# Performance work log

Hardware: AMD Instinct MI355X
Metric: run time of the kernel (lower is better)

Reference implementation:

```python
import jax, jax.numpy as jnp
import numpy as np

N = 100000      # nodes
E = 1600000     # edges (before self loops)
F_IN = 128
HID = 32
H = 4
OUT = 32
NEG_SLOPE = 0.2


def setup_inputs() -> dict:
    key = jax.random.key(0)
    ks = jax.random.split(key, 10)
    x = jax.random.normal(ks[0], (N, F_IN), jnp.float32)
    edge_index = jax.random.randint(ks[1], (2, E), 0, N, jnp.int32)
    s1 = 1.0 / np.sqrt(F_IN)
    s2 = 1.0 / np.sqrt(H * HID)
    W1 = jax.random.normal(ks[2], (F_IN, H * HID), jnp.float32) * s1
    a_src1 = jax.random.normal(ks[3], (H, HID), jnp.float32) * 0.1
    a_dst1 = jax.random.normal(ks[4], (H, HID), jnp.float32) * 0.1
    b1 = jnp.zeros((H * HID,), jnp.float32)
    W2 = jax.random.normal(ks[5], (H * HID, OUT), jnp.float32) * s2
    a_src2 = jax.random.normal(ks[6], (1, OUT), jnp.float32) * 0.1
    a_dst2 = jax.random.normal(ks[7], (1, OUT), jnp.float32) * 0.1
    b2 = jnp.zeros((OUT,), jnp.float32)
    return {"x": x, "edge_index": edge_index, "W1": W1, "a_src1": a_src1,
            "a_dst1": a_dst1, "b1": b1, "W2": W2, "a_src2": a_src2,
            "a_dst2": a_dst2, "b2": b2}


def gat_conv(x, src, dst, W, a_src, a_dst, b, heads, out_ch):
    # PyG GATConv (concat=True) with self loops already appended to src/dst.
    n = x.shape[0]
    h = (x @ W).reshape(n, heads, out_ch)                 # [N,H,C]
    alpha_s = jnp.sum(h * a_src, axis=-1)                 # [N,H]
    alpha_d = jnp.sum(h * a_dst, axis=-1)                 # [N,H]
    e = jax.nn.leaky_relu(alpha_s[src] + alpha_d[dst], NEG_SLOPE)  # [E',H]
    # segment softmax over destination nodes (self loops => every segment nonempty)
    emax = jax.ops.segment_max(e, dst, num_segments=n)
    ex = jnp.exp(e - emax[dst])
    denom = jax.ops.segment_sum(ex, dst, num_segments=n)
    alpha = ex / denom[dst]                               # [E',H]
    msg = h[src] * alpha[:, :, None]                      # [E',H,C]
    out = jax.ops.segment_sum(msg, dst, num_segments=n)   # [N,H,C]
    return out.reshape(n, heads * out_ch) + b


def reference(x, edge_index, W1, a_src1, a_dst1, b1, W2, a_src2, a_dst2, b2):
    loops = jnp.arange(N, dtype=edge_index.dtype)
    src = jnp.concatenate([edge_index[0], loops])
    dst = jnp.concatenate([edge_index[1], loops])
    h = gat_conv(x, src, dst, W1, a_src1, a_dst1, b1, H, HID)
    h = jax.nn.relu(h)                                    # dropout: eval mode, no-op
    out = gat_conv(h, src, dst, W2, a_src2, a_dst2, b2, 1, OUT)
    return out
```

## Files before the change

kernel.cpp:

```cpp
#include <hip/hip_runtime.h>
#include <hip/hip_fp16.h>

#define NEG 0.2f
#define EPB 4096
#define BSH 6
#define SLOT 48
#define CAP 1280
#define KBMAX 1664
#define SRCBITS 20
#define SRCMASK 0xFFFFFu

typedef _Float16 half8 __attribute__((ext_vector_type(8)));
typedef float f32x4 __attribute__((ext_vector_type(4)));

__device__ inline __half2 pun_h2(float f) { union { float f; __half2 h; } u; u.f = f; return u.h; }
__device__ inline float pun_f(__half2 h) { union { float f; __half2 h; } u; u.h = h; return u.f; }

__global__ void k_prep(const float* __restrict__ W1, const float* __restrict__ W2,
                       half8* __restrict__ Wp, half8* __restrict__ W2p,
                       int* __restrict__ gcount, int KB) {
    int b = blockIdx.x;
    if (b < 8) {
        int u = b * 256 + threadIdx.x;
        int s = u >> 9, tn = (u >> 6) & 7, lane = u & 63;
        int quad = lane >> 4, c = lane & 15;
        half8 v;
#pragma unroll
        for (int j = 0; j < 8; ++j)
            v[j] = (_Float16)W1[(s * 32 + quad * 8 + j) * 128 + tn * 16 + c];
        Wp[u] = v;
    } else if (b < 10) {
        int u = (b - 8) * 256 + threadIdx.x;
        int n = u >> 8, s = (u >> 6) & 3, lane = u & 63;
        int quad = lane >> 4, c = lane & 15;
        half8 v;
#pragma unroll
        for (int j = 0; j < 8; ++j)
            v[j] = (_Float16)W2[(s * 32 + quad * 8 + j) * 32 + n * 16 + c];
        W2p[u] = v;
    } else {
        int i = (b - 10) * 256 + threadIdx.x;
        if (i < KB) gcount[i] = 0;
    }
}

__global__ __launch_bounds__(256) void k_pA(const float* __restrict__ x,
                                            const half8* __restrict__ Wp,
                                            const float* __restrict__ a_s,
                                            const float* __restrict__ a_d,
                                            __half* __restrict__ h1h,
                                            float* __restrict__ as1,
                                            float* __restrict__ ad1, int N,
                                            const int* __restrict__ srcp,
                                            const int* __restrict__ dstp,
                                            int* __restrict__ gcount,
                                            unsigned* __restrict__ ebuf,
                                            int E, int KB, int ngemm) {
    __shared__ _Float16 xa[64][136];
    __shared__ int lh[KBMAX];
    int t = threadIdx.x;

    if (blockIdx.x >= ngemm) {
        int blk = blockIdx.x - ngemm;
        int base0 = blk * EPB;
        int ss[16], dd[16];
#pragma unroll
        for (int j = 0; j < 16; ++j) {
            int i = base0 + j * 256 + t;
            if (i < E) { ss[j] = srcp[i]; dd[j] = dstp[i]; } else dd[j] = -1;
        }
        for (int i = t; i < KB; i += 256) lh[i] = 0;
        __syncthreads();
#pragma unroll
        for (int j = 0; j < 16; ++j)
            if (dd[j] >= 0) atomicAdd(&lh[dd[j] >> BSH], 1);
        __syncthreads();
        for (int b = t; b < KB; b += 256) {
            int c = lh[b];
            if (c > 0) lh[b] = atomicAdd(&gcount[b], c);
        }
        __syncthreads();
#pragma unroll
        for (int j = 0; j < 16; ++j) {
            if (dd[j] >= 0) {
                int b = dd[j] >> BSH;
                int pos = atomicAdd(&lh[b], 1);
                ebuf[(size_t)b * CAP + pos] =
                    (unsigned)ss[j] | ((unsigned)(dd[j] & 63) << SRCBITS);
            }
        }
        return;
    }

    int row0 = blockIdx.x * 64;
    {
        int row = t >> 2;
        int col0 = (t & 3) * 32;
        int gr = row0 + row;
        const float4* xsrc = (const float4*)&x[(size_t)gr * 128 + col0];
#pragma unroll
        for (int m = 0; m < 4; ++m) {
            float4 p0, p1;
            if (gr < N) { p0 = xsrc[m * 2]; p1 = xsrc[m * 2 + 1]; }
            else { p0 = float4{0,0,0,0}; p1 = float4{0,0,0,0}; }
            half8 v;
            v[0] = (_Float16)p0.x; v[1] = (_Float16)p0.y;
            v[2] = (_Float16)p0.z; v[3] = (_Float16)p0.w;
            v[4] = (_Float16)p1.x; v[5] = (_Float16)p1.y;
            v[6] = (_Float16)p1.z; v[7] = (_Float16)p1.w;
            *(half8*)&xa[row][col0 + m * 8] = v;
        }
    }
    __syncthreads();

    int w = t >> 6;
    int lane = t & 63;
    int quad = lane >> 4, c = lane & 15;

    f32x4 acc[8];
#pragma unroll
    for (int i = 0; i < 8; ++i) acc[i] = f32x4{0, 0, 0, 0};

#pragma unroll
    for (int s = 0; s < 4; ++s) {
        half8 a = *(const half8*)&xa[w * 16 + c][s * 32 + quad * 8];
#pragma unroll
        for (int tn = 0; tn < 8; ++tn) {
            half8 b = Wp[(s * 8 + tn) * 64 + lane];
            acc[tn] = __builtin_amdgcn_mfma_f32_16x16x32_f16(a, b, acc[tn], 0, 0, 0);
        }
    }

    float asv[8], adv[8];
#pragma unroll
    for (int tn = 0; tn < 8; ++tn) { asv[tn] = a_s[tn * 16 + c]; adv[tn] = a_d[tn * 16 + c]; }
#pragma unroll
    for (int r = 0; r < 4; ++r) {
        int gr = row0 + w * 16 + quad * 4 + r;
#pragma unroll
        for (int h = 0; h < 4; ++h) {
            float ps = acc[2*h][r] * asv[2*h] + acc[2*h+1][r] * asv[2*h+1];
            float pd = acc[2*h][r] * adv[2*h] + acc[2*h+1][r] * adv[2*h+1];
            ps += __shfl_xor(ps, 1); ps += __shfl_xor(ps, 2);
            ps += __shfl_xor(ps, 4); ps += __shfl_xor(ps, 8);
            pd += __shfl_xor(pd, 1); pd += __shfl_xor(pd, 2);
            pd += __shfl_xor(pd, 4); pd += __shfl_xor(pd, 8);
            if (c == 0 && gr < N) { as1[gr * 4 + h] = ps; ad1[gr * 4 + h] = pd; }
        }
    }

    __syncthreads();
#pragma unroll
    for (int tn = 0; tn < 8; ++tn)
#pragma unroll
        for (int r = 0; r < 4; ++r)
            xa[w * 16 + quad * 4 + r][tn * 16 + c] = (_Float16)acc[tn][r];
    __syncthreads();
    {
        int row = t >> 2;
        int seg = t & 3;
        int gr = row0 + row;
        if (gr < N) {
            float4* gp = (float4*)&h1h[(size_t)gr * 128 + seg * 32];
#pragma unroll
            for (int i = 0; i < 4; ++i)
                gp[i] = *(float4*)&xa[row][seg * 32 + i * 8];
        }
    }
}

__global__ __launch_bounds__(256) void k_aggC(const unsigned* __restrict__ ebuf,
                                              const int* __restrict__ gcount,
                                              const __half* __restrict__ h1h,
                                              const float* __restrict__ as1,
                                              const float* __restrict__ ad1,
                                              const float* __restrict__ b1,
                                              const half8* __restrict__ W2p,
                                              const float* __restrict__ asw,
                                              const float* __restrict__ adw,
                                              __half* __restrict__ h2h,
                                              float* __restrict__ as2,
                                              float* __restrict__ ad2, int N) {
    __shared__ int lcnt[64];
    __shared__ int lcsr[64 * SLOT];
    __shared__ _Float16 stg[4][16][136];
    int t = threadIdx.x;
    int b = blockIdx.x, d0 = b << BSH;

    if (t < 64) lcnt[t] = 0;
    __syncthreads();

    int ecnt = gcount[b];
    const unsigned* eb = &ebuf[(size_t)b * CAP];
    for (int i = t; i < ecnt; i += 256) {
        unsigned e = eb[i];
        int li = e >> SRCBITS;
        int r = atomicAdd(&lcnt[li], 1);
        lcsr[li * SLOT + r] = (int)(e & SRCMASK);
    }
    __syncthreads();

    int w = t >> 6, lane = t & 63;
    int q = lane >> 5, c4 = lane & 31;
    int head4 = c4 >> 3;
    const __half2* hp = (const __half2*)h1h;
    float4 bv4 = *(const float4*)&b1[4 * c4];

    for (int i = 0; i < 8; ++i) {
        int li = w * 16 + 2 * i + q;
        int dst = d0 + li;
        bool valid = dst < N;
        int cnt = valid ? lcnt[li] : 0;
        int cbase = li * SLOT;
        float adv = valid ? ad1[dst * 4 + head4] : 0.f;
        float a0 = 0.f, a1 = 0.f, a2 = 0.f, a3 = 0.f, den = 0.f;
        float g0 = 0.f, g1 = 0.f, g2 = 0.f, g3 = 0.f, dn2 = 0.f;
        if (valid) {
            float es = as1[dst * 4 + head4] + adv;
            es = es > 0.f ? es : NEG * es;
            float xs = __expf(es);
            float2 vv = *(const float2*)&hp[(size_t)dst * 64 + 2 * c4];
            float2 f01 = __half22float2(pun_h2(vv.x));
            float2 f23 = __half22float2(pun_h2(vv.y));
            a0 = xs * f01.x; a1 = xs * f01.y; a2 = xs * f23.x; a3 = xs * f23.y;
            den = xs;
        }
        int e = 0;
        for (; e + 7 < cnt; e += 8) {
            int si[8];
#pragma unroll
            for (int j = 0; j < 8; ++j) si[j] = lcsr[cbase + e + j];
            float ej[8];
#pragma unroll
            for (int j = 0; j < 8; ++j) ej[j] = as1[si[j] * 4 + head4];
            float2 vj[8];
#pragma unroll
            for (int j = 0; j < 8; ++j) vj[j] = *(const float2*)&hp[(size_t)si[j] * 64 + 2 * c4];
#pragma unroll
            for (int j = 0; j < 8; ++j) {
                float ee = ej[j] + adv;
                ee = ee > 0.f ? ee : NEG * ee;
                float xw = __expf(ee);
                float2 f01 = __half22float2(pun_h2(vj[j].x));
                float2 f23 = __half22float2(pun_h2(vj[j].y));
                if ((j & 1) == 0) {
                    a0 += xw * f01.x; a1 += xw * f01.y;
                    a2 += xw * f23.x; a3 += xw * f23.y;
                    den += xw;
                } else {
                    g0 += xw * f01.x; g1 += xw * f01.y;
                    g2 += xw * f23.x; g3 += xw * f23.y;
                    dn2 += xw;
                }
            }
        }
        for (; e + 3 < cnt; e += 4) {
            int si[4];
#pragma unroll
            for (int j = 0; j < 4; ++j) si[j] = lcsr[cbase + e + j];
            float ej[4];
#pragma unroll
            for (int j = 0; j < 4; ++j) ej[j] = as1[si[j] * 4 + head4];
            float2 vj[4];
#pragma unroll
            for (int j = 0; j < 4; ++j) vj[j] = *(const float2*)&hp[(size_t)si[j] * 64 + 2 * c4];
#pragma unroll
            for (int j = 0; j < 4; ++j) {
                float ee = ej[j] + adv;
                ee = ee > 0.f ? ee : NEG * ee;
                float xw = __expf(ee);
                float2 f01 = __half22float2(pun_h2(vj[j].x));
                float2 f23 = __half22float2(pun_h2(vj[j].y));
                if ((j & 1) == 0) {
                    a0 += xw * f01.x; a1 += xw * f01.y;
                    a2 += xw * f23.x; a3 += xw * f23.y;
                    den += xw;
                } else {
                    g0 += xw * f01.x; g1 += xw * f01.y;
                    g2 += xw * f23.x; g3 += xw * f23.y;
                    dn2 += xw;
                }
            }
        }
        for (; e < cnt; ++e) {
            int s0 = lcsr[cbase + e];
            float e0v = as1[s0 * 4 + head4] + adv;
            float2 vv = *(const float2*)&hp[(size_t)s0 * 64 + 2 * c4];
            e0v = e0v > 0.f ? e0v : NEG * e0v;  float x0 = __expf(e0v);
            float2 f01 = __half22float2(pun_h2(vv.x));
            float2 f23 = __half22float2(pun_h2(vv.y));
            g0 += x0 * f01.x; g1 += x0 * f01.y;
            g2 += x0 * f23.x; g3 += x0 * f23.y;
            dn2 += x0;
        }
        a0 += g0; a1 += g1; a2 += g2; a3 += g3; den += dn2;
        float inv = valid ? 1.f / den : 0.f;
        float o0 = a0 * inv + bv4.x;
        float o1 = a1 * inv + bv4.y;
        float o2 = a2 * inv + bv4.z;
        float o3 = a3 * inv + bv4.w;
        o0 = o0 > 0.f ? o0 : 0.f;
        o1 = o1 > 0.f ? o1 : 0.f;
        o2 = o2 > 0.f ? o2 : 0.f;
        o3 = o3 > 0.f ? o3 : 0.f;
        float2 st;
        st.x = pun_f(__floats2half2_rn(o0, o1));
        st.y = pun_f(__floats2half2_rn(o2, o3));
        *(float2*)&stg[w][2 * i + q][4 * c4] = st;
    }

    int quad = lane >> 4, c16 = lane & 15;
    half8 bf[2][4];
#pragma unroll
    for (int n = 0; n < 2; ++n)
#pragma unroll
        for (int s = 0; s < 4; ++s) bf[n][s] = W2p[(n * 4 + s) * 64 + lane];
    float asw0 = asw[c16], asw1 = asw[16 + c16];
    float adw0 = adw[c16], adw1 = adw[16 + c16];

    f32x4 am0 = {0, 0, 0, 0}, am1 = {0, 0, 0, 0};
#pragma unroll
    for (int s = 0; s < 4; ++s) {
        half8 a = *(const half8*)&stg[w][c16][s * 32 + quad * 8];
        am0 = __builtin_amdgcn_mfma_f32_16x16x32_f16(a, bf[0][s], am0, 0, 0, 0);
        am1 = __builtin_amdgcn_mfma_f32_16x16x32_f16(a, bf[1][s], am1, 0, 0, 0);
    }
#pragma unroll
    for (int r = 0; r < 4; ++r) {
        int dst = d0 + w * 16 + quad * 4 + r;
        float ps = am0[r] * asw0 + am1[r] * asw1;
        float pd = am0[r] * adw0 + am1[r] * adw1;
        ps += __shfl_xor(ps, 1); ps += __shfl_xor(ps, 2);
        ps += __shfl_xor(ps, 4); ps += __shfl_xor(ps, 8);
        pd += __shfl_xor(pd, 1); pd += __shfl_xor(pd, 2);
        pd += __shfl_xor(pd, 4); pd += __shfl_xor(pd, 8);
        if (dst < N) {
            h2h[(size_t)dst * 32 + c16]      = __float2half_rn(am0[r]);
            h2h[(size_t)dst * 32 + 16 + c16] = __float2half_rn(am1[r]);
            if (c16 == 0) { as2[dst] = ps; ad2[dst] = pd; }
        }
    }
}

__global__ __launch_bounds__(256) void k_agg2(const unsigned* __restrict__ ebuf,
                                              const int* __restrict__ gcount,
                                              const __half* __restrict__ h2h,
                                              const float* __restrict__ as2,
                                              const float* __restrict__ ad2,
                                              const float* __restrict__ b2,
                                              float* __restrict__ out, int N) {
    __shared__ int lcnt[64];
    __shared__ int lcsr[64 * SLOT];
    int t = threadIdx.x;
    int b = blockIdx.x, d0 = b << BSH;

    if (t < 64) lcnt[t] = 0;
    __syncthreads();

    int ecnt = gcount[b];
    const unsigned* eb = &ebuf[(size_t)b * CAP];
    for (int i = t; i < ecnt; i += 256) {
        unsigned e = eb[i];
        int li = e >> SRCBITS;
        int r = atomicAdd(&lcnt[li], 1);
        lcsr[li * SLOT + r] = (int)(e & SRCMASK);
    }
    __syncthreads();

    int w = t >> 6, lane = t & 63;
    int g = lane >> 4, c2 = lane & 15;
    const __half2* h2 = (const __half2*)h2h;
    float2 bv;
    bv.x = b2[2 * c2]; bv.y = b2[2 * c2 + 1];

    for (int i = 0; i < 4; ++i) {
        int li = w * 16 + i * 4 + g;
        int dst = d0 + li;
        bool valid = dst < N;
        int cnt = valid ? lcnt[li] : 0;
        int cbase = li * SLOT;
        float adv = valid ? ad2[dst] : 0.f;
        float aA0 = 0.f, aA1 = 0.f, dA = 0.f;
        float aB0 = 0.f, aB1 = 0.f, dB = 0.f;
        if (valid) {
            float es = as2[dst] + adv;
            es = es > 0.f ? es : NEG * es;
            float xs = __expf(es);
            float2 hv = __half22float2(h2[(size_t)dst * 16 + c2]);
            aA0 = xs * hv.x; aA1 = xs * hv.y; dA = xs;
        }
        int e = 0;
        for (; e + 15 < cnt; e += 16) {
            int si[16];
#pragma unroll
            for (int j = 0; j < 16; ++j) si[j] = lcsr[cbase + e + j];
            float ej[16];
#pragma unroll
            for (int j = 0; j < 16; ++j) ej[j] = as2[si[j]];
            __half2 vj[16];
#pragma unroll
            for (int j = 0; j < 16; ++j) vj[j] = h2[(size_t)si[j] * 16 + c2];
#pragma unroll
            for (int j = 0; j < 16; ++j) {
                float ee = ej[j] + adv;
                ee = ee > 0.f ? ee : NEG * ee;
                float xw = __expf(ee);
                float2 hv = __half22float2(vj[j]);
                if ((j & 1) == 0) { aA0 += xw * hv.x; aA1 += xw * hv.y; dA += xw; }
                else              { aB0 += xw * hv.x; aB1 += xw * hv.y; dB += xw; }
            }
        }
        for (; e + 7 < cnt; e += 8) {
            int si[8];
#pragma unroll
            for (int j = 0; j < 8; ++j) si[j] = lcsr[cbase + e + j];
            float ej[8];
#pragma unroll
            for (int j = 0; j < 8; ++j) ej[j] = as2[si[j]];
            __half2 vj[8];
#pragma unroll
            for (int j = 0; j < 8; ++j) vj[j] = h2[(size_t)si[j] * 16 + c2];
#pragma unroll
            for (int j = 0; j < 8; ++j) {
                float ee = ej[j] + adv;
                ee = ee > 0.f ? ee : NEG * ee;
                float xw = __expf(ee);
                float2 hv = __half22float2(vj[j]);
                if ((j & 1) == 0) { aA0 += xw * hv.x; aA1 += xw * hv.y; dA += xw; }
                else              { aB0 += xw * hv.x; aB1 += xw * hv.y; dB += xw; }
            }
        }
        for (; e + 3 < cnt; e += 4) {
            int si[4];
#pragma unroll
            for (int j = 0; j < 4; ++j) si[j] = lcsr[cbase + e + j];
            float ej[4];
#pragma unroll
            for (int j = 0; j < 4; ++j) ej[j] = as2[si[j]];
            __half2 vj[4];
#pragma unroll
            for (int j = 0; j < 4; ++j) vj[j] = h2[(size_t)si[j] * 16 + c2];
#pragma unroll
            for (int j = 0; j < 4; ++j) {
                float ee = ej[j] + adv;
                ee = ee > 0.f ? ee : NEG * ee;
                float xw = __expf(ee);
                float2 hv = __half22float2(vj[j]);
                if ((j & 1) == 0) { aA0 += xw * hv.x; aA1 += xw * hv.y; dA += xw; }
                else              { aB0 += xw * hv.x; aB1 += xw * hv.y; dB += xw; }
            }
        }
        for (; e < cnt; ++e) {
            int s0 = lcsr[cbase + e];
            float e0 = as2[s0] + adv;
            float2 hv = __half22float2(h2[(size_t)s0 * 16 + c2]);
            e0 = e0 > 0.f ? e0 : NEG * e0;  float x0 = __expf(e0);
            aB0 += x0 * hv.x; aB1 += x0 * hv.y; dB += x0;
        }
        if (valid) {
            float invd = 1.f / (dA + dB);
            float2 o;
            o.x = (aA0 + aB0) * invd + bv.x;
            o.y = (aA1 + aB1) * invd + bv.y;
            *(float2*)&out[(size_t)dst * 32 + 2 * c2] = o;
        }
    }
}

extern "C" void kernel_launch(void* const* d_in, const int* in_sizes, int n_in,
                              void* d_out, int out_size, void* d_ws, size_t ws_size,
                              hipStream_t stream) {
    const float* x     = (const float*)d_in[0];
    const int*   ei    = (const int*)d_in[1];
    const float* W1    = (const float*)d_in[2];
    const float* as_w1 = (const float*)d_in[3];
    const float* ad_w1 = (const float*)d_in[4];
    const float* b1    = (const float*)d_in[5];
    const float* W2    = (const float*)d_in[6];
    const float* as_w2 = (const float*)d_in[7];
    const float* ad_w2 = (const float*)d_in[8];
    const float* b2    = (const float*)d_in[9];
    float* out = (float*)d_out;

    int N  = in_sizes[0] / 128;
    int E  = in_sizes[1] / 2;
    const int* srcp = ei;
    const int* dstp = ei + E;

    int KB     = (N + 63) >> BSH;
    int nblkB  = (E + EPB - 1) / EPB;
    int ngemm  = (N + 63) / 64;

    char* p = (char*)d_ws;
    auto alloc = [&](size_t bytes) -> char* {
        char* r = p;
        p += (bytes + 255) & ~(size_t)255;
        return r;
    };
    __half*   h1h    = (__half*)alloc((size_t)N * 128 * 2);
    float*    as1    = (float*)alloc((size_t)N * 4 * 4);
    float*    ad1    = (float*)alloc((size_t)N * 4 * 4);
    __half*   h2h    = (__half*)alloc((size_t)N * 32 * 2);
    float*    as2    = (float*)alloc((size_t)N * 4);
    float*    ad2    = (float*)alloc((size_t)N * 4);
    half8*    Wp     = (half8*)alloc(2048 * 16);
    half8*    W2p    = (half8*)alloc(512 * 16);
    int*      gcount = (int*)alloc((size_t)KB * 4);
    unsigned* ebuf   = (unsigned*)alloc((size_t)KB * CAP * 4);

    k_prep<<<10 + (KB + 255) / 256, 256, 0, stream>>>(W1, W2, Wp, W2p, gcount, KB);
    k_pA<<<ngemm + nblkB, 256, 0, stream>>>(x, Wp, as_w1, ad_w1, h1h, as1, ad1, N,
                                            srcp, dstp, gcount, ebuf, E, KB, ngemm);
    k_aggC<<<KB, 256, 0, stream>>>(ebuf, gcount, h1h, as1, ad1, b1,
                                   W2p, as_w2, ad_w2, h2h, as2, ad2, N);
    k_agg2<<<KB, 256, 0, stream>>>(ebuf, gcount, h2h, as2, ad2, b2, out, N);
}
```

Baseline: 268.1 us.

## Fold attention vectors into W1 via extra MFMA and store h1 in permuted channel layout

```diff
diff --git a/kernel.cpp b/kernel.cpp
--- a/kernel.cpp
+++ b/kernel.cpp
@@ -16,8 +16,12 @@
 __device__ inline __half2 pun_h2(float f) { union { float f; __half2 h; } u; u.f = f; return u.h; }
 __device__ inline float pun_f(__half2 h) { union { float f; __half2 h; } u; u.h = h; return u.f; }
 
+
 __global__ void k_prep(const float* __restrict__ W1, const float* __restrict__ W2,
+                       const float* __restrict__ a_s, const float* __restrict__ a_d,
+                       const float* __restrict__ b1,
                        half8* __restrict__ Wp, half8* __restrict__ W2p,
+                       half8* __restrict__ Wa, float* __restrict__ b1p,
                        int* __restrict__ gcount, int KB) {
     int b = blockIdx.x;
     if (b < 8) {
@@ -35,19 +39,40 @@
         int quad = lane >> 4, c = lane & 15;
         half8 v;
 #pragma unroll
-        for (int j = 0; j < 8; ++j)
-            v[j] = (_Float16)W2[(s * 32 + quad * 8 + j) * 32 + n * 16 + c];
+        for (int j = 0; j < 8; ++j) {
+            int p = s * 32 + quad * 8 + j;
+            int ch = ((p & 7) << 4) | (p >> 3);
+            v[j] = (_Float16)W2[ch * 32 + n * 16 + c];
+        }
         W2p[u] = v;
+    } else if (b == 10) {
+        int u = threadIdx.x;
+        int s = u >> 6, lane = u & 63;
+        int quad = lane >> 4, c = lane & 15;
+        half8 v;
+#pragma unroll
+        for (int j = 0; j < 8; ++j) {
+            int k = s * 32 + quad * 8 + j;
+            float acc = 0.f;
+            if (c < 8) {
+                int h = c & 3;
+                const float* av = (c < 4) ? a_s : a_d;
+                for (int cc = 0; cc < 32; ++cc)
+                    acc += W1[k * 128 + h * 32 + cc] * av[h * 32 + cc];
+            }
+            v[j] = (_Float16)acc;
+        }
+        Wa[u] = v;
+        if (u < 128) b1p[u] = b1[((u & 7) << 4) | (u >> 3)];
     } else {
-        int i = (b - 10) * 256 + threadIdx.x;
+        int i = (b - 11) * 256 + threadIdx.x;
         if (i < KB) gcount[i] = 0;
     }
 }
 
 __global__ __launch_bounds__(256) void k_pA(const float* __restrict__ x,
                                             const half8* __restrict__ Wp,
-                                            const float* __restrict__ a_s,
-                                            const float* __restrict__ a_d,
+                                            const half8* __restrict__ Wa,
                                             __half* __restrict__ h1h,
                                             float* __restrict__ as1,
                                             float* __restrict__ ad1, int N,
@@ -117,9 +142,14 @@
     int lane = t & 63;
     int quad = lane >> 4, c = lane & 15;
 
+    half8 wa[4];
+#pragma unroll
+    for (int s = 0; s < 4; ++s) wa[s] = Wa[s * 64 + lane];
+
     f32x4 acc[8];
 #pragma unroll
     for (int i = 0; i < 8; ++i) acc[i] = f32x4{0, 0, 0, 0};
+    f32x4 accA = f32x4{0, 0, 0, 0};
 
 #pragma unroll
     for (int s = 0; s < 4; ++s) {
@@ -129,42 +159,19 @@
             half8 b = Wp[(s * 8 + tn) * 64 + lane];
             acc[tn] = __builtin_amdgcn_mfma_f32_16x16x32_f16(a, b, acc[tn], 0, 0, 0);
         }
-    }
-
-    float asv[8], adv[8];
-#pragma unroll
-    for (int tn = 0; tn < 8; ++tn) { asv[tn] = a_s[tn * 16 + c]; adv[tn] = a_d[tn * 16 + c]; }
+        accA = __builtin_amdgcn_mfma_f32_16x16x32_f16(a, wa[s], accA, 0, 0, 0);
+    }
+
 #pragma unroll
     for (int r = 0; r < 4; ++r) {
         int gr = row0 + w * 16 + quad * 4 + r;
-#pragma unroll
-        for (int h = 0; h < 4; ++h) {
-            float ps = acc[2*h][r] * asv[2*h] + acc[2*h+1][r] * asv[2*h+1];
-            float pd = acc[2*h][r] * adv[2*h] + acc[2*h+1][r] * adv[2*h+1];
-            ps += __shfl_xor(ps, 1); ps += __shfl_xor(ps, 2);
-            ps += __shfl_xor(ps, 4); ps += __shfl_xor(ps, 8);
-            pd += __shfl_xor(pd, 1); pd += __shfl_xor(pd, 2);
-            pd += __shfl_xor(pd, 4); pd += __shfl_xor(pd, 8);
-            if (c == 0 && gr < N) { as1[gr * 4 + h] = ps; ad1[gr * 4 + h] = pd; }
-        }
-    }
-
-    __syncthreads();
-#pragma unroll
-    for (int tn = 0; tn < 8; ++tn)
-#pragma unroll
-        for (int r = 0; r < 4; ++r)
-            xa[w * 16 + quad * 4 + r][tn * 16 + c] = (_Float16)acc[tn][r];
-    __syncthreads();
-    {
-        int row = t >> 2;
-        int seg = t & 3;
-        int gr = row0 + row;
         if (gr < N) {
-            float4* gp = (float4*)&h1h[(size_t)gr * 128 + seg * 32];
-#pragma unroll
-            for (int i = 0; i < 4; ++i)
-                gp[i] = *(float4*)&xa[row][seg * 32 + i * 8];
+            half8 v;
+#pragma unroll
+            for (int k = 0; k < 8; ++k) v[k] = (_Float16)acc[k][r];
+            *(half8*)&h1h[(size_t)gr * 128 + c * 8] = v;
+            if (c < 4)      as1[gr * 4 + c] = accA[r];
+            else if (c < 8) ad1[gr * 4 + (c - 4)] = accA[r];
         }
     }
 }
@@ -206,51 +213,58 @@
     const __half2* hp = (const __half2*)h1h;
     float4 bv4 = *(const float4*)&b1[4 * c4];
 
+    int hA = ((4 * c4) & 7) >> 1;
+    int hB = hA + 1;
+
     for (int i = 0; i < 8; ++i) {
         int li = w * 16 + 2 * i + q;
         int dst = d0 + li;
         bool valid = dst < N;
         int cnt = valid ? lcnt[li] : 0;
         int cbase = li * SLOT;
-        float adv = valid ? ad1[dst * 4 + head4] : 0.f;
-        float a0 = 0.f, a1 = 0.f, a2 = 0.f, a3 = 0.f, den = 0.f;
-        float g0 = 0.f, g1 = 0.f, g2 = 0.f, g3 = 0.f, dn2 = 0.f;
+        float advA = valid ? ad1[dst * 4 + hA] : 0.f;
+        float advB = valid ? ad1[dst * 4 + hB] : 0.f;
+        float a0 = 0.f, a1 = 0.f, a2 = 0.f, a3 = 0.f, denA = 0.f, denB = 0.f;
+        float g0 = 0.f, g1 = 0.f, g2 = 0.f, g3 = 0.f, dnA2 = 0.f, dnB2 = 0.f;
         if (valid) {
-            float es = as1[dst * 4 + head4] + adv;
-            es = es > 0.f ? es : NEG * es;
-            float xs = __expf(es);
+            float esA = as1[dst * 4 + hA] + advA;
+            float esB = as1[dst * 4 + hB] + advB;
+            esA = esA > 0.f ? esA : NEG * esA;
+            esB = esB > 0.f ? esB : NEG * esB;
+            float xsA = __expf(esA), xsB = __expf(esB);
             float2 vv = *(const float2*)&hp[(size_t)dst * 64 + 2 * c4];
             float2 f01 = __half22float2(pun_h2(vv.x));
             float2 f23 = __half22float2(pun_h2(vv.y));
-            a0 = xs * f01.x; a1 = xs * f01.y; a2 = xs * f23.x; a3 = xs * f23.y;
-            den = xs;
+            a0 = xsA * f01.x; a1 = xsA * f01.y; a2 = xsB * f23.x; a3 = xsB * f23.y;
+            denA = xsA; denB = xsB;
         }
         int e = 0;
         for (; e + 7 < cnt; e += 8) {
             int si[8];
 #pragma unroll
             for (int j = 0; j < 8; ++j) si[j] = lcsr[cbase + e + j];
-            float ej[8];
-#pragma unroll
-            for (int j = 0; j < 8; ++j) ej[j] = as1[si[j] * 4 + head4];
+            float ejA[8], ejB[8];
+#pragma unroll
+            for (int j = 0; j < 8; ++j) { ejA[j] = as1[si[j] * 4 + hA]; ejB[j] = as1[si[j] * 4 + hB]; }
             float2 vj[8];
 #pragma unroll
             for (int j = 0; j < 8; ++j) vj[j] = *(const float2*)&hp[(size_t)si[j] * 64 + 2 * c4];
 #pragma unroll
             for (int j = 0; j < 8; ++j) {
-                float ee = ej[j] + adv;
-                ee = ee > 0.f ? ee : NEG * ee;
-                float xw = __expf(ee);
+                float eeA = ejA[j] + advA, eeB = ejB[j] + advB;
+                eeA = eeA > 0.f ? eeA : NEG * eeA;
+                eeB = eeB > 0.f ? eeB : NEG * eeB;
+                float xwA = __expf(eeA), xwB = __expf(eeB);
                 float2 f01 = __half22float2(pun_h2(vj[j].x));
                 float2 f23 = __half22float2(pun_h2(vj[j].y));
                 if ((j & 1) == 0) {
-                    a0 += xw * f01.x; a1 += xw * f01.y;
-                    a2 += xw * f23.x; a3 += xw * f23.y;
-                    den += xw;
+                    a0 += xwA * f01.x; a1 += xwA * f01.y;
+                    a2 += xwB * f23.x; a3 += xwB * f23.y;
+                    denA += xwA; denB += xwB;
                 } else {
-                    g0 += xw * f01.x; g1 += xw * f01.y;
-                    g2 += xw * f23.x; g3 += xw * f23.y;
-                    dn2 += xw;
+                    g0 += xwA * f01.x; g1 += xwA * f01.y;
+                    g2 += xwB * f23.x; g3 += xwB * f23.y;
+                    dnA2 += xwA; dnB2 += xwB;
                 }
             }
         }
@@ -258,47 +272,52 @@
             int si[4];
 #pragma unroll
             for (int j = 0; j < 4; ++j) si[j] = lcsr[cbase + e + j];
-            float ej[4];
-#pragma unroll
-            for (int j = 0; j < 4; ++j) ej[j] = as1[si[j] * 4 + head4];
+            float ejA[4], ejB[4];
+#pragma unroll
+            for (int j = 0; j < 4; ++j) { ejA[j] = as1[si[j] * 4 + hA]; ejB[j] = as1[si[j] * 4 + hB]; }
             float2 vj[4];
 #pragma unroll
             for (int j = 0; j < 4; ++j) vj[j] = *(const float2*)&hp[(size_t)si[j] * 64 + 2 * c4];
 #pragma unroll
             for (int j = 0; j < 4; ++j) {
-                float ee = ej[j] + adv;
-                ee = ee > 0.f ? ee : NEG * ee;
-                float xw = __expf(ee);
+                float eeA = ejA[j] + advA, eeB = ejB[j] + advB;
+                eeA = eeA > 0.f ? eeA : NEG * eeA;
+                eeB = eeB > 0.f ? eeB : NEG * eeB;
+                float xwA = __expf(eeA), xwB = __expf(eeB);
                 float2 f01 = __half22float2(pun_h2(vj[j].x));
                 float2 f23 = __half22float2(pun_h2(vj[j].y));
                 if ((j & 1) == 0) {
-                    a0 += xw * f01.x; a1 += xw * f01.y;
-                    a2 += xw * f23.x; a3 += xw * f23.y;
-                    den += xw;
+                    a0 += xwA * f01.x; a1 += xwA * f01.y;
+                    a2 += xwB * f23.x; a3 += xwB * f23.y;
+                    denA += xwA; denB += xwB;
                 } else {
-                    g0 += xw * f01.x; g1 += xw * f01.y;
-                    g2 += xw * f23.x; g3 += xw * f23.y;
-                    dn2 += xw;
+                    g0 += xwA * f01.x; g1 += xwA * f01.y;
+                    g2 += xwB * f23.x; g3 += xwB * f23.y;
+                    dnA2 += xwA; dnB2 += xwB;
                 }
             }
         }
         for (; e < cnt; ++e) {
             int s0 = lcsr[cbase + e];
-            float e0v = as1[s0 * 4 + head4] + adv;
+            float e0A = as1[s0 * 4 + hA] + advA;
+            float e0B = as1[s0 * 4 + hB] + advB;
             float2 vv = *(const float2*)&hp[(size_t)s0 * 64 + 2 * c4];
-            e0v = e0v > 0.f ? e0v : NEG * e0v;  float x0 = __expf(e0v);
+            e0A = e0A > 0.f ? e0A : NEG * e0A;  float x0A = __expf(e0A);
+            e0B = e0B > 0.f ? e0B : NEG * e0B;  float x0B = __expf(e0B);
             float2 f01 = __half22float2(pun_h2(vv.x));
             float2 f23 = __half22float2(pun_h2(vv.y));
-            g0 += x0 * f01.x; g1 += x0 * f01.y;
-            g2 += x0 * f23.x; g3 += x0 * f23.y;
-            dn2 += x0;
-        }
-        a0 += g0; a1 += g1; a2 += g2; a3 += g3; den += dn2;
-        float inv = valid ? 1.f / den : 0.f;
-        float o0 = a0 * inv + bv4.x;
-        float o1 = a1 * inv + bv4.y;
-        float o2 = a2 * inv + bv4.z;
-        float o3 = a3 * inv + bv4.w;
+            g0 += x0A * f01.x; g1 += x0A * f01.y;
+            g2 += x0B * f23.x; g3 += x0B * f23.y;
+            dnA2 += x0A; dnB2 += x0B;
+        }
+        a0 += g0; a1 += g1; a2 += g2; a3 += g3;
+        denA += dnA2; denB += dnB2;
+        float invA = valid ? 1.f / denA : 0.f;
+        float invB = valid ? 1.f / denB : 0.f;
+        float o0 = a0 * invA + bv4.x;
+        float o1 = a1 * invA + bv4.y;
+        float o2 = a2 * invB + bv4.z;
+        float o3 = a3 * invB + bv4.w;
         o0 = o0 > 0.f ? o0 : 0.f;
         o1 = o1 > 0.f ? o1 : 0.f;
         o2 = o2 > 0.f ? o2 : 0.f;
@@ -505,13 +524,16 @@
     float*    ad2    = (float*)alloc((size_t)N * 4);
     half8*    Wp     = (half8*)alloc(2048 * 16);
     half8*    W2p    = (half8*)alloc(512 * 16);
+    half8*    Wa     = (half8*)alloc(256 * 16);
+    float*    b1p    = (float*)alloc(128 * 4);
     int*      gcount = (int*)alloc((size_t)KB * 4);
     unsigned* ebuf   = (unsigned*)alloc((size_t)KB * CAP * 4);
 
-    k_prep<<<10 + (KB + 255) / 256, 256, 0, stream>>>(W1, W2, Wp, W2p, gcount, KB);
-    k_pA<<<ngemm + nblkB, 256, 0, stream>>>(x, Wp, as_w1, ad_w1, h1h, as1, ad1, N,
+    k_prep<<<11 + (KB + 255) / 256, 256, 0, stream>>>(W1, W2, as_w1, ad_w1, b1,
+                                                      Wp, W2p, Wa, b1p, gcount, KB);
+    k_pA<<<ngemm + nblkB, 256, 0, stream>>>(x, Wp, Wa, h1h, as1, ad1, N,
                                             srcp, dstp, gcount, ebuf, E, KB, ngemm);
-    k_aggC<<<KB, 256, 0, stream>>>(ebuf, gcount, h1h, as1, ad1, b1,
+    k_aggC<<<KB, 256, 0, stream>>>(ebuf, gcount, h1h, as1, ad1, b1p,
                                    W2p, as_w2, ad_w2, h2h, as2, ad2, N);
     k_agg2<<<KB, 256, 0, stream>>>(ebuf, gcount, h2h, as2, ad2, b2, out, N);
 }
```

New measurement: 280.7 us. +4.7%, slower.

## Fold attention vectors into an extra MFMA and enlarge edge-bucketing blocks

Applied to the files above, without the earlier changes.

```diff
diff --git a/kernel.cpp b/kernel.cpp
--- a/kernel.cpp
+++ b/kernel.cpp
@@ -2,7 +2,7 @@
 #include <hip/hip_fp16.h>
 
 #define NEG 0.2f
-#define EPB 4096
+#define EPB 16384
 #define BSH 6
 #define SLOT 48
 #define CAP 1280
@@ -17,7 +17,9 @@
 __device__ inline float pun_f(__half2 h) { union { float f; __half2 h; } u; u.h = h; return u.f; }
 
 __global__ void k_prep(const float* __restrict__ W1, const float* __restrict__ W2,
+                       const float* __restrict__ a_s, const float* __restrict__ a_d,
                        half8* __restrict__ Wp, half8* __restrict__ W2p,
+                       half8* __restrict__ Wa,
                        int* __restrict__ gcount, int KB) {
     int b = blockIdx.x;
     if (b < 8) {
@@ -38,16 +40,33 @@
         for (int j = 0; j < 8; ++j)
             v[j] = (_Float16)W2[(s * 32 + quad * 8 + j) * 32 + n * 16 + c];
         W2p[u] = v;
+    } else if (b == 10) {
+        int u = threadIdx.x;
+        int s = u >> 6, lane = u & 63;
+        int quad = lane >> 4, c = lane & 15;
+        half8 v;
+#pragma unroll
+        for (int j = 0; j < 8; ++j) {
+            int k = s * 32 + quad * 8 + j;
+            float acc = 0.f;
+            if (c < 8) {
+                int h = c & 3;
+                const float* av = (c < 4) ? a_s : a_d;
+                for (int cc = 0; cc < 32; ++cc)
+                    acc += W1[k * 128 + h * 32 + cc] * av[h * 32 + cc];
+            }
+            v[j] = (_Float16)acc;
+        }
+        Wa[u] = v;
     } else {
-        int i = (b - 10) * 256 + threadIdx.x;
+        int i = (b - 11) * 256 + threadIdx.x;
         if (i < KB) gcount[i] = 0;
     }
 }
 
 __global__ __launch_bounds__(256) void k_pA(const float* __restrict__ x,
                                             const half8* __restrict__ Wp,
-                                            const float* __restrict__ a_s,
-                                            const float* __restrict__ a_d,
+                                            const half8* __restrict__ Wa,
                                             __half* __restrict__ h1h,
                                             float* __restrict__ as1,
                                             float* __restrict__ ad1, int N,
@@ -55,44 +74,47 @@
                                             const int* __restrict__ dstp,
                                             int* __restrict__ gcount,
                                             unsigned* __restrict__ ebuf,
-                                            int E, int KB, int ngemm) {
+                                            int E, int KB, int nblkB) {
     __shared__ _Float16 xa[64][136];
     __shared__ int lh[KBMAX];
     int t = threadIdx.x;
 
-    if (blockIdx.x >= ngemm) {
-        int blk = blockIdx.x - ngemm;
-        int base0 = blk * EPB;
-        int ss[16], dd[16];
-#pragma unroll
-        for (int j = 0; j < 16; ++j) {
-            int i = base0 + j * 256 + t;
-            if (i < E) { ss[j] = srcp[i]; dd[j] = dstp[i]; } else dd[j] = -1;
-        }
+    if (blockIdx.x < nblkB) {
+        int base0 = blockIdx.x * EPB;
         for (int i = t; i < KB; i += 256) lh[i] = 0;
         __syncthreads();
-#pragma unroll
-        for (int j = 0; j < 16; ++j)
-            if (dd[j] >= 0) atomicAdd(&lh[dd[j] >> BSH], 1);
+        for (int ch = 0; ch < 4; ++ch) {
+            int cb = base0 + ch * 4096;
+#pragma unroll
+            for (int j = 0; j < 16; ++j) {
+                int i = cb + j * 256 + t;
+                if (i < E) atomicAdd(&lh[dstp[i] >> BSH], 1);
+            }
+        }
         __syncthreads();
         for (int b = t; b < KB; b += 256) {
             int c = lh[b];
             if (c > 0) lh[b] = atomicAdd(&gcount[b], c);
         }
         __syncthreads();
-#pragma unroll
-        for (int j = 0; j < 16; ++j) {
-            if (dd[j] >= 0) {
-                int b = dd[j] >> BSH;
-                int pos = atomicAdd(&lh[b], 1);
-                ebuf[(size_t)b * CAP + pos] =
-                    (unsigned)ss[j] | ((unsigned)(dd[j] & 63) << SRCBITS);
+        for (int ch = 0; ch < 4; ++ch) {
+            int cb = base0 + ch * 4096;
+#pragma unroll
+            for (int j = 0; j < 16; ++j) {
+                int i = cb + j * 256 + t;
+                if (i < E) {
+                    int d = dstp[i];
+                    int b = d >> BSH;
+                    int pos = atomicAdd(&lh[b], 1);
+                    ebuf[(size_t)b * CAP + pos] =
+                        (unsigned)srcp[i] | ((unsigned)(d & 63) << SRCBITS);
+                }
             }
         }
         return;
     }
 
-    int row0 = blockIdx.x * 64;
+    int row0 = (blockIdx.x - nblkB) * 64;
     {
         int row = t >> 2;
         int col0 = (t & 3) * 32;
@@ -117,9 +139,14 @@
     int lane = t & 63;
     int quad = lane >> 4, c = lane & 15;
 
+    half8 wa[4];
+#pragma unroll
+    for (int s = 0; s < 4; ++s) wa[s] = Wa[s * 64 + lane];
+
     f32x4 acc[8];
 #pragma unroll
     for (int i = 0; i < 8; ++i) acc[i] = f32x4{0, 0, 0, 0};
+    f32x4 accA = f32x4{0, 0, 0, 0};
 
 #pragma unroll
     for (int s = 0; s < 4; ++s) {
@@ -129,23 +156,15 @@
             half8 b = Wp[(s * 8 + tn) * 64 + lane];
             acc[tn] = __builtin_amdgcn_mfma_f32_16x16x32_f16(a, b, acc[tn], 0, 0, 0);
         }
-    }
-
-    float asv[8], adv[8];
-#pragma unroll
-    for (int tn = 0; tn < 8; ++tn) { asv[tn] = a_s[tn * 16 + c]; adv[tn] = a_d[tn * 16 + c]; }
+        accA = __builtin_amdgcn_mfma_f32_16x16x32_f16(a, wa[s], accA, 0, 0, 0);
+    }
+
 #pragma unroll
     for (int r = 0; r < 4; ++r) {
         int gr = row0 + w * 16 + quad * 4 + r;
-#pragma unroll
-        for (int h = 0; h < 4; ++h) {
-            float ps = acc[2*h][r] * asv[2*h] + acc[2*h+1][r] * asv[2*h+1];
-            float pd = acc[2*h][r] * adv[2*h] + acc[2*h+1][r] * adv[2*h+1];
-            ps += __shfl_xor(ps, 1); ps += __shfl_xor(ps, 2);
-            ps += __shfl_xor(ps, 4); ps += __shfl_xor(ps, 8);
-            pd += __shfl_xor(pd, 1); pd += __shfl_xor(pd, 2);
-            pd += __shfl_xor(pd, 4); pd += __shfl_xor(pd, 8);
-            if (c == 0 && gr < N) { as1[gr * 4 + h] = ps; ad1[gr * 4 + h] = pd; }
+        if (gr < N) {
+            if (c < 4)      as1[gr * 4 + c] = accA[r];
+            else if (c < 8) ad1[gr * 4 + (c - 4)] = accA[r];
         }
     }
 
@@ -505,12 +524,14 @@
     float*    ad2    = (float*)alloc((size_t)N * 4);
     half8*    Wp     = (half8*)alloc(2048 * 16);
     half8*    W2p    = (half8*)alloc(512 * 16);
+    half8*    Wa     = (half8*)alloc(256 * 16);
     int*      gcount = (int*)alloc((size_t)KB * 4);
     unsigned* ebuf   = (unsigned*)alloc((size_t)KB * CAP * 4);
 
-    k_prep<<<10 + (KB + 255) / 256, 256, 0, stream>>>(W1, W2, Wp, W2p, gcount, KB);
-    k_pA<<<ngemm + nblkB, 256, 0, stream>>>(x, Wp, as_w1, ad_w1, h1h, as1, ad1, N,
-                                            srcp, dstp, gcount, ebuf, E, KB, ngemm);
+    k_prep<<<11 + (KB + 255) / 256, 256, 0, stream>>>(W1, W2, as_w1, ad_w1,
+                                                      Wp, W2p, Wa, gcount, KB);
+    k_pA<<<nblkB + ngemm, 256, 0, stream>>>(x, Wp, Wa, h1h, as1, ad1, N,
+                                            srcp, dstp, gcount, ebuf, E, KB, nblkB);
     k_aggC<<<KB, 256, 0, stream>>>(ebuf, gcount, h1h, as1, ad1, b1,
                                    W2p, as_w2, ad_w2, h2h, as2, ad2, N);
     k_agg2<<<KB, 256, 0, stream>>>(ebuf, gcount, h2h, as2, ad2, b2, out, N);
```

Measured after the change: 315.6 us. 1.18x slower.
